# Optimization experiments

Hardware: AMD Instinct MI355X
Metric: run time of the kernel (lower is better)

Reference implementation:

```python
import jax, jax.numpy as jnp
import numpy as np
from jax import lax

BATCH, SEQ, IN_DIM, STATE, OUT_DIM = 8, 4096, 256, 256, 256


def setup_inputs() -> dict:
    key = jax.random.key(0)
    kx, ka, kb, kc = jax.random.split(key, 4)
    x = jax.random.normal(kx, (BATCH, SEQ, IN_DIM), dtype=jnp.float32)
    # A initialized as randn normalized by its largest singular value (spectral norm)
    A_init = jax.random.normal(ka, (STATE, STATE), dtype=jnp.float32)
    s_max = jnp.linalg.svd(A_init, compute_uv=False)[0]
    A = A_init / (s_max + 1e-8)
    B = jax.random.normal(kb, (IN_DIM, STATE), dtype=jnp.float32) / IN_DIM
    C = jax.random.normal(kc, (STATE, OUT_DIM), dtype=jnp.float32) / STATE
    h0 = jnp.zeros((STATE,), dtype=jnp.float32)
    return {"x": x, "A": A, "B": B, "C": C, "h0": h0}


def reference(x, A, B, C, h0):
    # h_{t} = h_{t-1} @ A + x_t @ B ;  y_t = h_t @ C
    bsz = x.shape[0]
    xB = jnp.einsum('bsi,in->sbn', x, B)  # precompute input projections, time-major
    h_init = jnp.broadcast_to(h0, (bsz, h0.shape[0]))

    def step(h, xb_t):
        h = h @ A + xb_t
        return h, h

    _, hs = lax.scan(step, h_init, xB)  # hs: [S, B, N]
    y = jnp.einsum('sbn,no->bso', hs, C)  # [B, S, O]
    return y
```

## Files before the change

kernel.cpp:

```cpp
#include <hip/hip_runtime.h>


#define SEQ    4096
#define NBATCH 8
#define ND     256
#define CHUNK  8
#define NCHUNK 512
#define GSZ    16
#define NGRP   32
#define LOSC   2048.0f
#define LOINV  (1.0f/2048.0f)

typedef _Float16 fp16_t;
typedef __attribute__((ext_vector_type(8))) _Float16 f16x8;
typedef __attribute__((ext_vector_type(4))) _Float16 f16x4;
typedef __attribute__((ext_vector_type(4))) float f32x4;

__device__ __forceinline__ void pin(f16x8& x) { asm volatile("" : "+v"(x)); }

__global__ __launch_bounds__(64) void prep_frags3(
    const float* __restrict__ A, const float* __restrict__ B,
    const float* __restrict__ C,
    fp16_t* __restrict__ fAh, fp16_t* __restrict__ fAl,
    fp16_t* __restrict__ fBh, fp16_t* __restrict__ fBl,
    fp16_t* __restrict__ fCh, fp16_t* __restrict__ fCl) {
  const int which = blockIdx.x >> 7;
  const int blk   = blockIdx.x & 127;
  const float* M = (which == 0) ? A : (which == 1) ? B : C;
  fp16_t* hi = (which == 0) ? fAh : (which == 1) ? fBh : fCh;
  fp16_t* lo = (which == 0) ? fAl : (which == 1) ? fBl : fCl;
  const int lane = threadIdx.x;
  const int tile = blk >> 3, slice = blk & 7;
  const int n  = tile * 16 + (lane & 15);
  const int k0 = slice * 32 + (lane >> 4) * 8;
  f16x8 vh, vl;
  #pragma unroll
  for (int j = 0; j < 8; ++j) {
    const float v = M[(size_t)(k0 + j) * ND + n];
    const fp16_t h = (fp16_t)v;
    vh[j] = h;
    vl[j] = (fp16_t)((v - (float)h) * LOSC);
  }
  const size_t fo = ((size_t)blk * 64 + lane) * 8;
  *(f16x8*)&hi[fo] = vh;
  *(f16x8*)&lo[fo] = vl;
}

__global__ __launch_bounds__(64) void prep_frags2(
    const float* __restrict__ M0, const float* __restrict__ M1,
    fp16_t* __restrict__ h0p, fp16_t* __restrict__ l0p,
    fp16_t* __restrict__ h1p, fp16_t* __restrict__ l1p) {
  const int which = blockIdx.x >> 7;
  const int blk   = blockIdx.x & 127;
  const float* M = (which == 0) ? M0 : M1;
  fp16_t* hi = (which == 0) ? h0p : h1p;
  fp16_t* lo = (which == 0) ? l0p : l1p;
  const int lane = threadIdx.x;
  const int tile = blk >> 3, slice = blk & 7;
  const int n  = tile * 16 + (lane & 15);
  const int k0 = slice * 32 + (lane >> 4) * 8;
  f16x8 vh, vl;
  #pragma unroll
  for (int j = 0; j < 8; ++j) {
    const float v = M[(size_t)(k0 + j) * ND + n];
    const fp16_t h = (fp16_t)v;
    vh[j] = h;
    vl[j] = (fp16_t)((v - (float)h) * LOSC);
  }
  const size_t fo = ((size_t)blk * 64 + lane) * 8;
  *(f16x8*)&hi[fo] = vh;
  *(f16x8*)&lo[fo] = vl;
}

__global__ __launch_bounds__(1024, 2) void mfma_gemm(const float* __restrict__ X,
                                                     const fp16_t* __restrict__ Mhi,
                                                     const fp16_t* __restrict__ Mlo,
                                                     float* __restrict__ Out,
                                                     int mode) {
  const int m0   = blockIdx.x * 64;
  const int tid  = threadIdx.x;
  const int lane = tid & 63;
  const int w    = tid >> 6;
  const int br   = lane & 15;
  const int akg  = lane >> 4;

  __shared__ fp16_t Xh[32 * 512];
  __shared__ fp16_t Xl[32 * 512];
  char* Xhb = (char*)Xh;
  char* Xlb = (char*)Xl;

  #pragma unroll
  for (int pass = 0; pass < 2; ++pass) {
    const int tau = pass * 1024 + tid;
    const int row = tau >> 5;
    const int sub = tau & 31;
    const int s   = sub >> 2;
    const int ak  = sub & 3;
    const int m = m0 + row;
    const size_t in_row = (mode == 0)
        ? ((size_t)(m & 7) * SEQ + (m >> 3))
        : (size_t)m;
    const float* xp = &X[in_row * ND + s * 32 + ak * 8];
    const float4 x0 = *(const float4*)(xp);
    const float4 x1 = *(const float4*)(xp + 4);
    const float a[8] = {x0.x, x0.y, x0.z, x0.w, x1.x, x1.y, x1.z, x1.w};
    f16x8 vh, vl;
    #pragma unroll
    for (int j = 0; j < 8; ++j) {
      const fp16_t h = (fp16_t)a[j];
      vh[j] = h;
      vl[j] = (fp16_t)((a[j] - (float)h) * LOSC);
    }
    const int off = (((row >> 4) * 8 + s) << 10) +
                    (((ak << 4) | (row & 15)) ^ s) * 16;
    *(f16x8*)(Xhb + off) = vh;
    *(f16x8*)(Xlb + off) = vl;
  }

  f16x8 MH[8], ML[8];
  #pragma unroll
  for (int s = 0; s < 8; ++s) {
    const size_t fo = (((size_t)w * 8 + s) * 64 + lane) * 8;
    MH[s] = *(const f16x8*)&Mhi[fo];
    ML[s] = *(const f16x8*)&Mlo[fo];
    pin(MH[s]);
    pin(ML[s]);
  }
  __syncthreads();

  f32x4 accm[4], accl[4];
  #pragma unroll
  for (int mt = 0; mt < 4; ++mt) {
    accm[mt] = (f32x4)0.0f;
    accl[mt] = (f32x4)0.0f;
  }

  #pragma unroll
  for (int s = 0; s < 8; ++s) {
    #pragma unroll
    for (int mt = 0; mt < 4; ++mt) {
      const int byte = ((mt * 8 + s) << 10) + ((((akg << 4) | br) ^ s) << 4);
      const f16x8 bh = *(const f16x8*)(Xhb + byte);
      const f16x8 bl = *(const f16x8*)(Xlb + byte);
      accm[mt] = __builtin_amdgcn_mfma_f32_16x16x32_f16(MH[s], bh, accm[mt], 0, 0, 0);
      accl[mt] = __builtin_amdgcn_mfma_f32_16x16x32_f16(ML[s], bh, accl[mt], 0, 0, 0);
      accl[mt] = __builtin_amdgcn_mfma_f32_16x16x32_f16(MH[s], bl, accl[mt], 0, 0, 0);
    }
  }

  #pragma unroll
  for (int mt = 0; mt < 4; ++mt) {
    const int m = m0 + mt * 16 + br;
    const size_t out_row = (mode == 1)
        ? ((size_t)(m & 7) * SEQ + (m >> 3))
        : (size_t)m;
    float4 o;
    o.x = accm[mt][0] + accl[mt][0] * LOINV;
    o.y = accm[mt][1] + accl[mt][1] * LOINV;
    o.z = accm[mt][2] + accl[mt][2] * LOINV;
    o.w = accm[mt][3] + accl[mt][3] * LOINV;
    *(float4*)&Out[out_row * ND + w * 16 + akg * 4] = o;
  }
}

__global__ __launch_bounds__(1024, 2) void mfma_rscan(
    const fp16_t* __restrict__ Mh, const fp16_t* __restrict__ Ml,
    const float* __restrict__ Init,
    const float* In,
    float* OutEach,
    float* __restrict__ OutFinal,
    int nupd, int gstride, int nseq, int init_bcast, int entry_mode) {
  const int seq0 = blockIdx.x * 2;
  const int tid  = threadIdx.x;
  const int lane = tid & 63;
  const int w    = tid >> 6;
  const int br   = lane & 15;
  const int akg  = lane >> 4;

  __shared__ fp16_t hH[2][8 * 512];
  __shared__ fp16_t hL[2][8 * 512];

  {
    const int task = tid >> 1;
    const int half = tid & 1;
    const int row  = task & 15;
    const int s    = (task >> 4) & 7;
    const int ak   = task >> 7;
    const int sq = seq0 + (row >> 3);
    const int b  = row & 7;
    const int c0 = s * 32 + ak * 8 + half * 4;
    f32x4 v = (f32x4)0.0f;
    if (Init != nullptr && sq < nseq) {
      const size_t off = init_bcast ? (size_t)c0
                                    : ((size_t)sq * NBATCH + b) * ND + c0;
      v = *(const f32x4*)&Init[off];
      if (entry_mode && OutEach != nullptr)
        *(f32x4*)&OutEach[((size_t)sq * gstride * NBATCH + b) * ND + c0] = v;
    }
    f16x4 vh, vl;
    #pragma unroll
    for (int j = 0; j < 4; ++j) {
      const fp16_t h = (fp16_t)v[j];
      vh[j] = h;
      vl[j] = (fp16_t)((v[j] - (float)h) * LOSC);
    }
    const int off = (s << 10) + ((((ak << 4) | row) ^ s) << 4) + half * 8;
    *(f16x4*)((char*)hH[0] + off) = vh;
    *(f16x4*)((char*)hL[0] + off) = vl;
  }

  f16x8 AH[8], AL[8];
  #pragma unroll
  for (int s = 0; s < 8; ++s) {
    const size_t fo = (((size_t)w * 8 + s) * 64 + lane) * 8;
    AH[s] = *(const f16x8*)&Mh[fo];
    AL[s] = *(const f16x8*)&Ml[fo];
    pin(AH[s]);
    pin(AL[s]);
  }
  __syncthreads();

  const int sq   = seq0 + (br >> 3);
  const int b    = br & 7;
  const bool live = (sq < nseq);
  const int sqc  = live ? sq : (nseq - 1);
  const int col0 = w * 16 + akg * 4;

  int rdoff[8];
  #pragma unroll
  for (int s = 0; s < 8; ++s)
    rdoff[s] = (s << 10) + ((((akg << 4) | br) ^ s) << 4);
  const int sw   = col0 >> 5;
  const int akr  = (col0 >> 3) & 3;
  const int wroff = (sw << 10) + ((((akr << 4) | br) ^ sw) << 4) + (col0 & 7) * 2;

  f32x4 uv = *(const f32x4*)&In[((size_t)(sqc * gstride) * NBATCH + b) * ND + col0];
  f32x4 uvn;
  f32x4 res;
  int p = 0;
  for (int j = 0; j < nupd; ++j) {
    if (j + 1 < nupd)
      uvn = *(const f32x4*)&In[((size_t)(sqc * gstride + j + 1) * NBATCH + b) * ND + col0];
    const char* rH = (const char*)hH[p];
    const char* rL = (const char*)hL[p];
    f32x4 accm = uv, acclA = (f32x4)0.0f, acclB = (f32x4)0.0f;
    #pragma unroll
    for (int s = 0; s < 8; ++s) {
      const f16x8 bh = *(const f16x8*)(rH + rdoff[s]);
      const f16x8 bl = *(const f16x8*)(rL + rdoff[s]);
      accm  = __builtin_amdgcn_mfma_f32_16x16x32_f16(AH[s], bh, accm,  0, 0, 0);
      acclA = __builtin_amdgcn_mfma_f32_16x16x32_f16(AL[s], bh, acclA, 0, 0, 0);
      acclB = __builtin_amdgcn_mfma_f32_16x16x32_f16(AH[s], bl, acclB, 0, 0, 0);
    }
    #pragma unroll
    for (int r = 0; r < 4; ++r) res[r] = accm[r] + (acclA[r] + acclB[r]) * LOINV;
    {
      f16x4 vh, vl;
      #pragma unroll
      for (int r = 0; r < 4; ++r) {
        const fp16_t hh = (fp16_t)res[r];
        vh[r] = hh;
        vl[r] = (fp16_t)((res[r] - (float)hh) * LOSC);
      }
      *(f16x4*)((char*)hH[p ^ 1] + wroff) = vh;
      *(f16x4*)((char*)hL[p ^ 1] + wroff) = vl;
    }
    if (OutEach != nullptr && live) {
      const size_t pos = entry_mode ? (size_t)(sq * gstride + j + 1)
                                    : (size_t)(sq * gstride + j);
      *(f32x4*)&OutEach[(pos * NBATCH + b) * ND + col0] = res;
    }
    uv = uvn;
    p ^= 1;
    __syncthreads();
  }

  if (OutFinal != nullptr && live)
    *(f32x4*)&OutFinal[((size_t)sq * NBATCH + b) * ND + col0] = res;
}

__global__ __launch_bounds__(256) void gemm256(const float* __restrict__ X,
                                               const float* __restrict__ Y,
                                               float* __restrict__ Out) {
  const int m0 = blockIdx.x * 4;
  const int n  = threadIdx.x;
  __shared__ float Xs[ND][4];
  #pragma unroll
  for (int r = 0; r < 4; ++r) Xs[n][r] = X[(m0 + r) * ND + n];
  __syncthreads();
  float a0 = 0.f, a1 = 0.f, a2 = 0.f, a3 = 0.f;
  #pragma unroll 8
  for (int k = 0; k < ND; ++k) {
    const float yv = Y[k * ND + n];
    const float4 xv = *(const float4*)&Xs[k][0];
    a0 = fmaf(xv.x, yv, a0);
    a1 = fmaf(xv.y, yv, a1);
    a2 = fmaf(xv.z, yv, a2);
    a3 = fmaf(xv.w, yv, a3);
  }
  Out[(m0 + 0) * ND + n] = a0;
  Out[(m0 + 1) * ND + n] = a1;
  Out[(m0 + 2) * ND + n] = a2;
  Out[(m0 + 3) * ND + n] = a3;
}

extern "C" void kernel_launch(void* const* d_in, const int* in_sizes, int n_in,
                              void* d_out, int out_size, void* d_ws, size_t ws_size,
                              hipStream_t stream) {
  const float* x  = (const float*)d_in[0];
  const float* A  = (const float*)d_in[1];
  const float* Bm = (const float*)d_in[2];
  const float* Cm = (const float*)d_in[3];
  const float* h0 = (const float*)d_in[4];
  float* y = (float*)d_out;

  float* U    = (float*)d_ws;
  float* t0   = U + (size_t)SEQ * NBATCH * ND;
  float* t1   = t0 + ND * ND;
  float* A8   = t1 + ND * ND;
  float* A128 = A8 + ND * ND;
  float* E    = A128 + ND * ND;
  float* Sg   = E + (size_t)NCHUNK * NBATCH * ND;
  float* G    = Sg + (size_t)NGRP * NBATCH * ND;
  float* Hc   = G + (size_t)NGRP * NBATCH * ND;
  fp16_t* fA_hi = (fp16_t*)(Hc + (size_t)NCHUNK * NBATCH * ND);
  fp16_t* fA_lo = fA_hi + ND * ND;
  fp16_t* fB_hi = fA_lo + ND * ND;
  fp16_t* fB_lo = fB_hi + ND * ND;
  fp16_t* fC_hi = fB_lo + ND * ND;
  fp16_t* fC_lo = fC_hi + ND * ND;
  fp16_t* fA8_hi   = (fp16_t*)t0;
  fp16_t* fA8_lo   = fA8_hi + ND * ND;
  fp16_t* fA128_hi = (fp16_t*)t1;
  fp16_t* fA128_lo = fA128_hi + ND * ND;

  prep_frags3<<<384, 64, 0, stream>>>(A, Bm, Cm, fA_hi, fA_lo, fB_hi, fB_lo,
                                      fC_hi, fC_lo);

  gemm256<<<64, 256, 0, stream>>>(A,  A,  t0);
  gemm256<<<64, 256, 0, stream>>>(t0, t0, t1);
  gemm256<<<64, 256, 0, stream>>>(t1, t1, A8);
  gemm256<<<64, 256, 0, stream>>>(A8, A8, t0);
  gemm256<<<64, 256, 0, stream>>>(t0, t0, t1);
  gemm256<<<64, 256, 0, stream>>>(t1, t1, t0);
  gemm256<<<64, 256, 0, stream>>>(t0, t0, A128);

  prep_frags2<<<256, 64, 0, stream>>>(A8, A128, fA8_hi, fA8_lo,
                                      fA128_hi, fA128_lo);

  mfma_gemm<<<512, 1024, 0, stream>>>(x, fB_hi, fB_lo, U, 0);

  mfma_rscan<<<NCHUNK / 2, 1024, 0, stream>>>(fA_hi, fA_lo, nullptr, U,
                                              nullptr, E, CHUNK, CHUNK,
                                              NCHUNK, 0, 0);

  mfma_rscan<<<NGRP / 2, 1024, 0, stream>>>(fA8_hi, fA8_lo, nullptr, E,
                                            nullptr, Sg, GSZ, GSZ, NGRP, 0, 0);

  mfma_rscan<<<1, 1024, 0, stream>>>(fA128_hi, fA128_lo, h0, Sg,
                                     G, nullptr, NGRP - 1, NGRP, 1, 1, 1);

  mfma_rscan<<<NGRP / 2, 1024, 0, stream>>>(fA8_hi, fA8_lo, G, E,
                                            Hc, nullptr, GSZ - 1, GSZ, NGRP,
                                            0, 1);

  mfma_rscan<<<NCHUNK / 2, 1024, 0, stream>>>(fA_hi, fA_lo, Hc, U,
                                              U, nullptr, CHUNK, CHUNK,
                                              NCHUNK, 0, 0);

  mfma_gemm<<<512, 1024, 0, stream>>>(U, fC_hi, fC_lo, y, 1);
}
```

Measured before the change: 269.5 us.

## Deepen chunked scan hierarchy to three levels of radix-8 with A^8, A^64, A^512

Replaces the two-level chunk scan (groups of 16 chunks, 32 groups) with a three-level radix-8 hierarchy using precomputed A^8, A^64 and A^512. The aim is to cut the longest sequential dependency chain: the serial top-level scan shrinks from 31 steps to 7, and each level now runs 8-step chains. The cost is two extra scan launches and two extra 256x256 matrix squarings for the higher powers. It also drops the empty asm register pins on the fragment loads, which leaves register allocation to the compiler.

Result: faster. 237.6 us (-11.8%).

```diff
diff --git a/kernel.cpp b/kernel.cpp
--- a/kernel.cpp
+++ b/kernel.cpp
@@ -6,8 +6,6 @@
 #define ND     256
 #define CHUNK  8
 #define NCHUNK 512
-#define GSZ    16
-#define NGRP   32
 #define LOSC   2048.0f
 #define LOINV  (1.0f/2048.0f)
 
@@ -15,8 +13,6 @@
 typedef __attribute__((ext_vector_type(8))) _Float16 f16x8;
 typedef __attribute__((ext_vector_type(4))) _Float16 f16x4;
 typedef __attribute__((ext_vector_type(4))) float f32x4;
-
-__device__ __forceinline__ void pin(f16x8& x) { asm volatile("" : "+v"(x)); }
 
 __global__ __launch_bounds__(64) void prep_frags3(
     const float* __restrict__ A, const float* __restrict__ B,
@@ -46,32 +42,6 @@
   *(f16x8*)&lo[fo] = vl;
 }
 
-__global__ __launch_bounds__(64) void prep_frags2(
-    const float* __restrict__ M0, const float* __restrict__ M1,
-    fp16_t* __restrict__ h0p, fp16_t* __restrict__ l0p,
-    fp16_t* __restrict__ h1p, fp16_t* __restrict__ l1p) {
-  const int which = blockIdx.x >> 7;
-  const int blk   = blockIdx.x & 127;
-  const float* M = (which == 0) ? M0 : M1;
-  fp16_t* hi = (which == 0) ? h0p : h1p;
-  fp16_t* lo = (which == 0) ? l0p : l1p;
-  const int lane = threadIdx.x;
-  const int tile = blk >> 3, slice = blk & 7;
-  const int n  = tile * 16 + (lane & 15);
-  const int k0 = slice * 32 + (lane >> 4) * 8;
-  f16x8 vh, vl;
-  #pragma unroll
-  for (int j = 0; j < 8; ++j) {
-    const float v = M[(size_t)(k0 + j) * ND + n];
-    const fp16_t h = (fp16_t)v;
-    vh[j] = h;
-    vl[j] = (fp16_t)((v - (float)h) * LOSC);
-  }
-  const size_t fo = ((size_t)blk * 64 + lane) * 8;
-  *(f16x8*)&hi[fo] = vh;
-  *(f16x8*)&lo[fo] = vl;
-}
-
 __global__ __launch_bounds__(1024, 2) void mfma_gemm(const float* __restrict__ X,
                                                      const fp16_t* __restrict__ Mhi,
                                                      const fp16_t* __restrict__ Mlo,
@@ -123,8 +93,6 @@
     const size_t fo = (((size_t)w * 8 + s) * 64 + lane) * 8;
     MH[s] = *(const f16x8*)&Mhi[fo];
     ML[s] = *(const f16x8*)&Mlo[fo];
-    pin(MH[s]);
-    pin(ML[s]);
   }
   __syncthreads();
 
@@ -215,8 +183,6 @@
     const size_t fo = (((size_t)w * 8 + s) * 64 + lane) * 8;
     AH[s] = *(const f16x8*)&Mh[fo];
     AL[s] = *(const f16x8*)&Ml[fo];
-    pin(AH[s]);
-    pin(AL[s]);
   }
   __syncthreads();
 
@@ -314,59 +280,70 @@
   const float* h0 = (const float*)d_in[4];
   float* y = (float*)d_out;
 
-  float* U    = (float*)d_ws;
-  float* t0   = U + (size_t)SEQ * NBATCH * ND;
-  float* t1   = t0 + ND * ND;
-  float* A8   = t1 + ND * ND;
-  float* A128 = A8 + ND * ND;
-  float* E    = A128 + ND * ND;
-  float* Sg   = E + (size_t)NCHUNK * NBATCH * ND;
-  float* G    = Sg + (size_t)NGRP * NBATCH * ND;
-  float* Hc   = G + (size_t)NGRP * NBATCH * ND;
-  fp16_t* fA_hi = (fp16_t*)(Hc + (size_t)NCHUNK * NBATCH * ND);
-  fp16_t* fA_lo = fA_hi + ND * ND;
-  fp16_t* fB_hi = fA_lo + ND * ND;
-  fp16_t* fB_lo = fB_hi + ND * ND;
-  fp16_t* fC_hi = fB_lo + ND * ND;
-  fp16_t* fC_lo = fC_hi + ND * ND;
-  fp16_t* fA8_hi   = (fp16_t*)t0;
-  fp16_t* fA8_lo   = fA8_hi + ND * ND;
-  fp16_t* fA128_hi = (fp16_t*)t1;
-  fp16_t* fA128_lo = fA128_hi + ND * ND;
+  float* U     = (float*)d_ws;
+  float* t0    = U + (size_t)SEQ * NBATCH * ND;
+  float* t1    = t0 + ND * ND;
+  float* A8f   = t1 + ND * ND;
+  float* A64f  = A8f + ND * ND;
+  float* A512f = A64f + ND * ND;
+  float* E     = A512f + ND * ND;
+  float* S1    = E + (size_t)NCHUNK * NBATCH * ND;
+  float* S2    = S1 + (size_t)64 * NBATCH * ND;
+  float* G3    = S2 + (size_t)8 * NBATCH * ND;
+  float* Hc2   = G3 + (size_t)8 * NBATCH * ND;
+  float* Hc    = Hc2 + (size_t)64 * NBATCH * ND;
+  fp16_t* fA_hi   = (fp16_t*)(Hc + (size_t)NCHUNK * NBATCH * ND);
+  fp16_t* fA_lo   = fA_hi + ND * ND;
+  fp16_t* fB_hi   = fA_lo + ND * ND;
+  fp16_t* fB_lo   = fB_hi + ND * ND;
+  fp16_t* fC_hi   = fB_lo + ND * ND;
+  fp16_t* fC_lo   = fC_hi + ND * ND;
+  fp16_t* fA8_hi  = fC_lo + ND * ND;
+  fp16_t* fA8_lo  = fA8_hi + ND * ND;
+  fp16_t* fA64_hi = fA8_lo + ND * ND;
+  fp16_t* fA64_lo = fA64_hi + ND * ND;
+  fp16_t* fA512_hi = fA64_lo + ND * ND;
+  fp16_t* fA512_lo = fA512_hi + ND * ND;
 
   prep_frags3<<<384, 64, 0, stream>>>(A, Bm, Cm, fA_hi, fA_lo, fB_hi, fB_lo,
                                       fC_hi, fC_lo);
 
-  gemm256<<<64, 256, 0, stream>>>(A,  A,  t0);
-  gemm256<<<64, 256, 0, stream>>>(t0, t0, t1);
-  gemm256<<<64, 256, 0, stream>>>(t1, t1, A8);
-  gemm256<<<64, 256, 0, stream>>>(A8, A8, t0);
-  gemm256<<<64, 256, 0, stream>>>(t0, t0, t1);
-  gemm256<<<64, 256, 0, stream>>>(t1, t1, t0);
-  gemm256<<<64, 256, 0, stream>>>(t0, t0, A128);
-
-  prep_frags2<<<256, 64, 0, stream>>>(A8, A128, fA8_hi, fA8_lo,
-                                      fA128_hi, fA128_lo);
+  gemm256<<<64, 256, 0, stream>>>(A,    A,    t0);
+  gemm256<<<64, 256, 0, stream>>>(t0,   t0,   t1);
+  gemm256<<<64, 256, 0, stream>>>(t1,   t1,   A8f);
+  gemm256<<<64, 256, 0, stream>>>(A8f,  A8f,  t0);
+  gemm256<<<64, 256, 0, stream>>>(t0,   t0,   t1);
+  gemm256<<<64, 256, 0, stream>>>(t1,   t1,   A64f);
+  gemm256<<<64, 256, 0, stream>>>(A64f, A64f, t0);
+  gemm256<<<64, 256, 0, stream>>>(t0,   t0,   t1);
+  gemm256<<<64, 256, 0, stream>>>(t1,   t1,   A512f);
+
+  prep_frags3<<<384, 64, 0, stream>>>(A8f, A64f, A512f,
+                                      fA8_hi, fA8_lo, fA64_hi, fA64_lo,
+                                      fA512_hi, fA512_lo);
 
   mfma_gemm<<<512, 1024, 0, stream>>>(x, fB_hi, fB_lo, U, 0);
 
   mfma_rscan<<<NCHUNK / 2, 1024, 0, stream>>>(fA_hi, fA_lo, nullptr, U,
-                                              nullptr, E, CHUNK, CHUNK,
-                                              NCHUNK, 0, 0);
-
-  mfma_rscan<<<NGRP / 2, 1024, 0, stream>>>(fA8_hi, fA8_lo, nullptr, E,
-                                            nullptr, Sg, GSZ, GSZ, NGRP, 0, 0);
-
-  mfma_rscan<<<1, 1024, 0, stream>>>(fA128_hi, fA128_lo, h0, Sg,
-                                     G, nullptr, NGRP - 1, NGRP, 1, 1, 1);
-
-  mfma_rscan<<<NGRP / 2, 1024, 0, stream>>>(fA8_hi, fA8_lo, G, E,
-                                            Hc, nullptr, GSZ - 1, GSZ, NGRP,
-                                            0, 1);
+                                              nullptr, E, 8, 8, NCHUNK, 0, 0);
+
+  mfma_rscan<<<32, 1024, 0, stream>>>(fA8_hi, fA8_lo, nullptr, E,
+                                      nullptr, S1, 8, 8, 64, 0, 0);
+
+  mfma_rscan<<<4, 1024, 0, stream>>>(fA64_hi, fA64_lo, nullptr, S1,
+                                     nullptr, S2, 8, 8, 8, 0, 0);
+
+  mfma_rscan<<<1, 1024, 0, stream>>>(fA512_hi, fA512_lo, h0, S2,
+                                     G3, nullptr, 7, 8, 1, 1, 1);
+
+  mfma_rscan<<<4, 1024, 0, stream>>>(fA64_hi, fA64_lo, G3, S1,
+                                     Hc2, nullptr, 7, 8, 8, 0, 1);
+
+  mfma_rscan<<<32, 1024, 0, stream>>>(fA8_hi, fA8_lo, Hc2, E,
+                                      Hc, nullptr, 7, 8, 64, 0, 1);
 
   mfma_rscan<<<NCHUNK / 2, 1024, 0, stream>>>(fA_hi, fA_lo, Hc, U,
-                                              U, nullptr, CHUNK, CHUNK,
-                                              NCHUNK, 0, 0);
+                                              U, nullptr, 8, 8, NCHUNK, 0, 0);
 
   mfma_gemm<<<512, 1024, 0, stream>>>(U, fC_hi, fC_lo, y, 1);
 }
```
